# Kernel optimization log

Measured on AMD Instinct MI355X. Metric: run time of the kernel, lower is better.

The kernel has to match this reference:

```python
import jax, jax.numpy as jnp
import numpy as np

EPS = 1e-5
N_NODES = 100000
N_EDGES = 1600000
IN_F, HID_F, OUT_F = 128, 128, 64


def setup_inputs() -> dict:
    key = jax.random.key(0)
    ks = jax.random.split(key, 8)
    def xavier(k, fan_in, fan_out):
        lim = float(np.sqrt(6.0 / (fan_in + fan_out)))
        return jax.random.uniform(k, (fan_in, fan_out), jnp.float32, -lim, lim)
    return {
        "features": jax.random.normal(ks[0], (N_NODES, IN_F), jnp.float32),
        "src": jax.random.randint(ks[1], (N_EDGES,), 0, N_NODES, jnp.int64 if jax.config.jax_enable_x64 else jnp.int32),
        "dst": jax.random.randint(ks[2], (N_EDGES,), 0, N_NODES, jnp.int64 if jax.config.jax_enable_x64 else jnp.int32),
        "W_self1": xavier(ks[3], IN_F, HID_F),
        "W_neigh1": xavier(ks[4], IN_F, HID_F),
        "b1": jnp.zeros((HID_F,), jnp.float32),
        "gamma1": jnp.ones((HID_F,), jnp.float32),
        "beta1": jnp.zeros((HID_F,), jnp.float32),
        "W_self2": xavier(ks[5], HID_F, OUT_F),
        "W_neigh2": xavier(ks[6], HID_F, OUT_F),
        "b2": jnp.zeros((OUT_F,), jnp.float32),
        "gamma2": jnp.ones((OUT_F,), jnp.float32),
        "beta2": jnp.zeros((OUT_F,), jnp.float32),
    }


def _sage_conv(h, src, dst, W_self, W_neigh, b, n_nodes):
    # mean aggregation of source-node features onto destination nodes
    agg = jax.ops.segment_sum(h[src], dst, num_segments=n_nodes)   # [N, d]
    deg = jax.ops.segment_sum(jnp.ones_like(dst, dtype=h.dtype), dst, num_segments=n_nodes)
    h_neigh = agg / jnp.maximum(deg, 1.0)[:, None]                  # zero-degree -> 0
    return h @ W_self + h_neigh @ W_neigh + b


def _batchnorm(h, gamma, beta):
    # training-mode BatchNorm1d: batch stats over node dim, biased variance
    mu = jnp.mean(h, axis=0)
    var = jnp.mean(jnp.square(h - mu), axis=0)
    return (h - mu) * jax.lax.rsqrt(var + EPS) * gamma + beta


def reference(features, src, dst, W_self1, W_neigh1, b1, gamma1, beta1,
              W_self2, W_neigh2, b2, gamma2, beta2):
    n = features.shape[0]
    h = _sage_conv(features, src, dst, W_self1, W_neigh1, b1, n)
    h = jax.nn.relu(_batchnorm(h, gamma1, beta1))
    h = _sage_conv(h, src, dst, W_self2, W_neigh2, b2, n)
    return _batchnorm(h, gamma2, beta2)
```

## Files before the change

kernel.cpp:

```cpp
#include <hip/hip_runtime.h>

#define EPS_BN 1e-5f
#define BINSHIFT 9
#define BINW 512
#define P_EPB 8192
#define LDS_CAP 10240
#define NREP 32

typedef __attribute__((ext_vector_type(8))) short short8;
typedef __attribute__((ext_vector_type(4))) float f32x4;

__device__ __forceinline__ unsigned short f2bf(float x) {
    unsigned int u = __float_as_uint(x);
    u += 0x7fffu + ((u >> 16) & 1u);
    return (unsigned short)(u >> 16);
}
__device__ __forceinline__ float bf2f(unsigned short h) {
    return __uint_as_float(((unsigned int)h) << 16);
}
__device__ __forceinline__ float bflo(unsigned u) { return __uint_as_float(u << 16); }
__device__ __forceinline__ float bfhi(unsigned u) { return __uint_as_float(u & 0xffff0000u); }
__device__ __forceinline__ float i8lo(unsigned short u) { return (float)(signed char)(u & 0xff); }
__device__ __forceinline__ float i8hi(unsigned short u) { return (float)(signed char)(u >> 8); }

__device__ __forceinline__ void scan512(int* a, int t) {
    for (int off = 1; off < 512; off <<= 1) {
        int v = (t >= off) ? a[t - off] : 0;
        __syncthreads();
        a[t] += v;
        __syncthreads();
    }
}
__device__ __forceinline__ void scan256(int* a, int t) {
    for (int off = 1; off < 256; off <<= 1) {
        int v = (t >= off) ? a[t - off] : 0;
        __syncthreads();
        a[t] += v;
        __syncthreads();
    }
}

__global__ __launch_bounds__(256) void prep_kernel(
    const float* __restrict__ Ws1, const float* __restrict__ Wn1,
    const float* __restrict__ Ws2, const float* __restrict__ Wn2,
    unsigned short* __restrict__ W1f, unsigned short* __restrict__ W2f,
    const int* __restrict__ dst, int* __restrict__ counts, int E, int NB, int wB) {
    int tid = threadIdx.x;
    if (blockIdx.x < wB) {
        int i = blockIdx.x * 256 + tid;
        if (i < 128 * 256) {
            int j = i & 7, L = (i >> 3) & 63, c = (i >> 9) & 15, kk = i >> 13;
            int k = kk * 32 + (L >> 4) * 8 + j;
            int col = c * 16 + (L & 15);
            float v = (col < 128) ? Ws1[k * 128 + col] : Wn1[k * 128 + (col - 128)];
            W1f[i] = f2bf(v);
        } else {
            int idx = i - 128 * 256;
            if (idx < 128 * 128) {
                int j = idx & 7, L = (idx >> 3) & 63, c = (idx >> 9) & 7, kk = idx >> 12;
                int k = kk * 32 + (L >> 4) * 8 + j;
                int col = c * 16 + (L & 15);
                float v = (col < 64) ? Ws2[k * 64 + col] : Wn2[k * 64 + (col - 64)];
                W2f[idx] = f2bf(v);
            }
        }
    } else {
        __shared__ int hist[512];
        int blk = blockIdx.x - wB;
        int e0 = blk * P_EPB, e1 = min(e0 + P_EPB, E);
        for (int b = tid; b < 512; b += 256) hist[b] = 0;
        __syncthreads();
        for (int e = e0 + tid; e < e1; e += 256) atomicAdd(&hist[dst[e] >> BINSHIFT], 1);
        __syncthreads();
        for (int b = tid; b < NB; b += 256) counts[blk * NB + b] = hist[b];
    }
}

__global__ __launch_bounds__(256) void p2a(const int* __restrict__ counts,
                                           int* __restrict__ segrel,
                                           int* __restrict__ tot, int NB, int NBLK) {
    __shared__ int s[256];
    int b = blockIdx.x, t = threadIdx.x;
    int v = (t < NBLK) ? counts[t * NB + b] : 0;
    s[t] = v;
    __syncthreads();
    scan256(s, t);
    if (t < NBLK) segrel[t * NB + b] = s[t] - v;
    if (t == 255) tot[b] = s[255];
}

__global__ __launch_bounds__(512) void p3_scatter(const int* __restrict__ src,
                                                  const int* __restrict__ dst,
                                                  const int* __restrict__ segrel,
                                                  const int* __restrict__ tot,
                                                  unsigned* __restrict__ epack,
                                                  int E, int NB) {
    __shared__ unsigned lp[P_EPB];
    __shared__ int hist[512];
    __shared__ int sBase[513];
    __shared__ int cursor[512];
    __shared__ int bbase[512];
    int t = threadIdx.x;
    int blk = blockIdx.x;
    int e0 = blk * P_EPB, e1 = min(e0 + P_EPB, E), m = e1 - e0;
    int tv = (t < NB) ? tot[t] : 0;
    bbase[t] = tv;
    __syncthreads();
    scan512(bbase, t);
    bbase[t] -= tv;
    hist[t] = 0;
    __syncthreads();
    for (int e = e0 + t; e < e1; e += 512) atomicAdd(&hist[dst[e] >> BINSHIFT], 1);
    __syncthreads();
    int h = hist[t];
    scan512(hist, t);
    int excl = hist[t] - h;
    sBase[t] = excl;
    cursor[t] = excl;
    if (t == 0) sBase[512] = m;
    __syncthreads();
    for (int e = e0 + t; e < e1; e += 512) {
        int d = dst[e];
        int pos = atomicAdd(&cursor[d >> BINSHIFT], 1);
        lp[pos] = ((unsigned)src[e] << BINSHIFT) | ((unsigned)d & (BINW - 1));
    }
    __syncthreads();
    for (int i = t; i < m; i += 512) {
        int lo = 0, hi = NB;
        while (hi - lo > 1) {
            int mid = (lo + hi) >> 1;
            if (sBase[mid] <= i) lo = mid; else hi = mid;
        }
        epack[bbase[lo] + segrel[blk * NB + lo] + (i - sBase[lo])] = lp[i];
    }
}

__global__ __launch_bounds__(512) void p4_csr(const unsigned* __restrict__ epack,
                                              const int* __restrict__ tot,
                                              int* __restrict__ row_start,
                                              int* __restrict__ cntg,
                                              float* __restrict__ inv_deg,
                                              int* __restrict__ csr_src, int N, int NB) {
    __shared__ int ncnt[512];
    __shared__ int cursor[512];
    __shared__ int bb[512];
    __shared__ int lsrc[LDS_CAP];
    int t = threadIdx.x;
    int b = blockIdx.x;
    int tv = (t < NB) ? tot[t] : 0;
    bb[t] = tv;
    __syncthreads();
    scan512(bb, t);
    int e1 = bb[b];
    int e0 = bb[b] - tot[b];
    int m = e1 - e0;
    int nbase = b << BINSHIFT;
    int nn = min(N - nbase, BINW);
    ncnt[t] = 0;
    __syncthreads();
    for (int i = e0 + t; i < e1; i += 512)
        atomicAdd(&ncnt[epack[i] & (BINW - 1)], 1);
    __syncthreads();
    int c = ncnt[t];
    scan512(ncnt, t);
    int excl = ncnt[t] - c;
    if (t < nn) {
        int node = nbase + t;
        row_start[node] = e0 + excl;
        cntg[node] = c;
        inv_deg[node] = 1.0f / fmaxf((float)c, 1.0f);
    }
    cursor[t] = excl;
    __syncthreads();
    for (int i = e0 + t; i < e1; i += 512) {
        unsigned v = epack[i];
        int pos = atomicAdd(&cursor[v & (BINW - 1)], 1);
        if (pos < LDS_CAP) lsrc[pos] = (int)(v >> BINSHIFT);
    }
    __syncthreads();
    int mm = min(m, LDS_CAP);
    for (int i = t; i < mm; i += 512) csr_src[e0 + i] = lsrc[i];
}

template <int MT, int MSELF, bool SELFBF, bool FUSEBN, bool AFP32>
__global__ __launch_bounds__(256) void gemm_dual(const unsigned short* __restrict__ Ab,
                                                 const float* __restrict__ Af,
                                                 const unsigned short* __restrict__ Wf,
                                                 float* __restrict__ YselfF,
                                                 unsigned short* __restrict__ YselfB,
                                                 signed char* __restrict__ Ynb8,
                                                 float* __restrict__ scl, int N,
                                                 const float* __restrict__ sums,
                                                 const float* __restrict__ gamma,
                                                 const float* __restrict__ beta,
                                                 float invN) {
    constexpr int K = 128;
    constexpr int NCT = MT / 16;
    constexpr int KS = K / 32;
    constexpr int MNB = MT - MSELF;
    constexpr int CSELF = MSELF / 16;
    __shared__ unsigned short Bl[KS * NCT * 64 * 8];
    __shared__ float ssc[128], ssh[128];

    for (int i = threadIdx.x; i < KS * NCT * 64; i += 256)
        ((short8*)Bl)[i] = ((const short8*)Wf)[i];
    if (FUSEBN && threadIdx.x < 128) {
        int c = threadIdx.x;
        float su = 0.f, sq = 0.f;
        for (int r = 0; r < NREP; r++) {
            su += sums[r * 256 + c];
            sq += sums[r * 256 + 128 + c];
        }
        float mu = su * invN;
        float var = sq * invN - mu * mu;
        float sc = gamma[c] * rsqrtf(var + EPS_BN);
        ssc[c] = sc;
        ssh[c] = beta[c] - mu * sc;
    }
    __syncthreads();

    int wv = threadIdx.x >> 6, lane = threadIdx.x & 63;
    int row0 = blockIdx.x * 128 + wv * 32;
    int m = lane & 15, quad = lane >> 4;

    short8 afrag[2][KS];
#pragma unroll
    for (int t = 0; t < 2; t++) {
        int arow = row0 + t * 16 + m;
        if (arow >= N) arow = N - 1;
#pragma unroll
        for (int kk = 0; kk < KS; kk++) {
            short8 raw;
            if (AFP32) {
                const float* ap = Af + (size_t)arow * K + quad * 8 + kk * 32;
                f32x4 a = *(const f32x4*)ap;
                f32x4 b = *(const f32x4*)(ap + 4);
#pragma unroll
                for (int j = 0; j < 4; j++) {
                    raw[j] = (short)f2bf(a[j]);
                    raw[4 + j] = (short)f2bf(b[j]);
                }
            } else {
                raw = *(const short8*)(Ab + (size_t)arow * K + quad * 8 + kk * 32);
            }
            if (FUSEBN) {
#pragma unroll
                for (int j = 0; j < 8; j++) {
                    int c = kk * 32 + quad * 8 + j;
                    float f = bf2f((unsigned short)raw[j]) * ssc[c] + ssh[c];
                    raw[j] = (short)f2bf(fmaxf(f, 0.f));
                }
            }
            afrag[t][kk] = raw;
        }
    }

    f32x4 acc[2][NCT];
#pragma unroll
    for (int t = 0; t < 2; t++)
        for (int c = 0; c < NCT; c++)
            for (int j = 0; j < 4; j++) acc[t][c][j] = 0.f;

#pragma unroll
    for (int kk = 0; kk < KS; kk++) {
#pragma unroll
        for (int c = 0; c < NCT; c++) {
            short8 bfrag = *(const short8*)&Bl[((kk * NCT + c) * 64 + lane) * 8];
#pragma unroll
            for (int t = 0; t < 2; t++)
                acc[t][c] = __builtin_amdgcn_mfma_f32_16x16x32_bf16(afrag[t][kk], bfrag,
                                                                    acc[t][c], 0, 0, 0);
        }
    }

#pragma unroll
    for (int t = 0; t < 2; t++) {
#pragma unroll
        for (int c = 0; c < CSELF; c++) {
            int colg = c * 16 + m;
#pragma unroll
            for (int r = 0; r < 4; r++) {
                int row = row0 + t * 16 + quad * 4 + r;
                if (row < N) {
                    float v = acc[t][c][r];
                    if (SELFBF)
                        YselfB[(size_t)row * MSELF + colg] = f2bf(v);
                    else
                        YselfF[(size_t)row * MSELF + colg] = v;
                }
            }
        }
#pragma unroll
        for (int r = 0; r < 4; r++) {
            float mx = 0.f;
#pragma unroll
            for (int c = CSELF; c < NCT; c++) mx = fmaxf(mx, fabsf(acc[t][c][r]));
#pragma unroll
            for (int off = 1; off < 16; off <<= 1) mx = fmaxf(mx, __shfl_xor(mx, off));
            int row = row0 + t * 16 + quad * 4 + r;
            float qs = 127.0f / fmaxf(mx, 1e-30f);
            if (row < N) {
                if (m == 0) scl[row] = mx * (1.0f / 127.0f);
#pragma unroll
                for (int c = CSELF; c < NCT; c++) {
                    int colg = c * 16 + m;
                    int q = __float2int_rn(acc[t][c][r] * qs);
                    Ynb8[(size_t)row * MNB + (colg - MSELF)] = (signed char)q;
                }
            }
        }
    }
}

__global__ __launch_bounds__(256) void agg_row128(const unsigned int* __restrict__ Sb,
                                                  const unsigned short* __restrict__ Tq,
                                                  const float* __restrict__ scl,
                                                  const int* __restrict__ row_start,
                                                  const int* __restrict__ cnt,
                                                  const float* __restrict__ inv_deg,
                                                  const int* __restrict__ csr_src,
                                                  const float* __restrict__ bias,
                                                  unsigned int* __restrict__ Out,
                                                  float* __restrict__ sums,
                                                  int N, int totalWaves) {
    int wv = threadIdx.x >> 6, lane = threadIdx.x & 63;
    int c = lane * 2;
    float bs0 = bias[c], bs1 = bias[c + 1];
    float S0 = 0.f, S1 = 0.f, Q0 = 0.f, Q1 = 0.f;

    int n = blockIdx.x * 4 + wv;
    int pStart = 0, pEc = 0, pIv = 0;
    float pInv = 0.f;
    if (n < N) {
        pStart = row_start[n];
        pEc = cnt[n];
        pInv = inv_deg[n];
        if (pEc > 0) pIv = csr_src[pStart + min(lane, min(pEc, 64) - 1)];
    }
    for (; n < N; n += totalWaves) {
        int start = pStart, ec = pEc, iv = pIv;
        float inv = pInv;
        unsigned su = Sb[(size_t)n * 64 + lane];
        int n2 = n + totalWaves;
        if (n2 < N) {
            pStart = row_start[n2];
            pEc = cnt[n2];
            pInv = inv_deg[n2];
            if (pEc > 0) pIv = csr_src[pStart + min(lane, min(pEc, 64) - 1)];
        }
        float a0 = 0.f, a1 = 0.f;
        for (int base = 0; base < ec; base += 64) {
            int ecc = min(ec - base, 64);
            if (base) iv = csr_src[start + base + min(lane, ecc - 1)];
            int e = 0;
            for (; e + 16 <= ecc; e += 16) {
                unsigned short u[16];
                float sc[16];
#pragma unroll
                for (int j = 0; j < 16; j++) {
                    int s = __builtin_amdgcn_readlane(iv, e + j);
                    u[j] = Tq[(size_t)s * 64 + lane];
                    sc[j] = scl[s];
                }
#pragma unroll
                for (int j = 0; j < 16; j++) {
                    a0 += sc[j] * i8lo(u[j]);
                    a1 += sc[j] * i8hi(u[j]);
                }
            }
            if (e + 8 <= ecc) {
                unsigned short u[8];
                float sc[8];
#pragma unroll
                for (int j = 0; j < 8; j++) {
                    int s = __builtin_amdgcn_readlane(iv, e + j);
                    u[j] = Tq[(size_t)s * 64 + lane];
                    sc[j] = scl[s];
                }
#pragma unroll
                for (int j = 0; j < 8; j++) {
                    a0 += sc[j] * i8lo(u[j]);
                    a1 += sc[j] * i8hi(u[j]);
                }
                e += 8;
            }
            if (e < ecc) {
                int r = ecc - e;
                unsigned short u[8];
                float sc[8];
#pragma unroll
                for (int j = 0; j < 8; j++) {
                    int s = __builtin_amdgcn_readlane(iv, min(e + j, ecc - 1));
                    u[j] = Tq[(size_t)s * 64 + lane];
                    sc[j] = scl[s];
                }
#pragma unroll
                for (int j = 0; j < 8; j++) {
                    if (j < r) {
                        a0 += sc[j] * i8lo(u[j]);
                        a1 += sc[j] * i8hi(u[j]);
                    }
                }
            }
        }
        float h0 = bflo(su) + a0 * inv + bs0;
        float h1 = bfhi(su) + a1 * inv + bs1;
        Out[(size_t)n * 64 + lane] = (unsigned)f2bf(h0) | ((unsigned)f2bf(h1) << 16);
        S0 += h0; Q0 += h0 * h0;
        S1 += h1; Q1 += h1 * h1;
    }
    __shared__ float ls[256];
    ls[threadIdx.x] = 0.f;
    __syncthreads();
    atomicAdd(&ls[c], S0);
    atomicAdd(&ls[c + 1], S1);
    atomicAdd(&ls[128 + c], Q0);
    atomicAdd(&ls[129 + c], Q1);
    __syncthreads();
    float* dstS = sums + (size_t)(blockIdx.x & (NREP - 1)) * 256;
    atomicAdd(&dstS[threadIdx.x], ls[threadIdx.x]);
}

__global__ __launch_bounds__(256) void agg_row64(const unsigned short* __restrict__ Tq,
                                                 const float* __restrict__ scl,
                                                 const int* __restrict__ row_start,
                                                 const int* __restrict__ cnt,
                                                 const float* __restrict__ inv_deg,
                                                 const int* __restrict__ csr_src,
                                                 const float* __restrict__ bias,
                                                 float* Self, float* __restrict__ sums,
                                                 int N, int totalWaves) {
    int wv = threadIdx.x >> 6, lane = threadIdx.x & 63;
    int g = lane >> 5, h = lane & 31;
    int c = h * 2;
    float bs0 = bias[c], bs1 = bias[c + 1];
    float S0 = 0.f, S1 = 0.f, Q0 = 0.f, Q1 = 0.f;

    int n = blockIdx.x * 4 + wv;
    int pStart = 0, pEc = 0, pIv = 0;
    if (n < N) {
        pStart = row_start[n];
        pEc = cnt[n];
        if (pEc > 0) pIv = csr_src[pStart + min(lane, min(pEc, 64) - 1)];
    }
    for (; n < N; n += totalWaves) {
        int start = pStart, ec = pEc, iv = pIv;
        float inv = inv_deg[n];
        int n2 = n + totalWaves;
        if (n2 < N) {
            pStart = row_start[n2];
            pEc = cnt[n2];
            if (pEc > 0) pIv = csr_src[pStart + min(lane, min(pEc, 64) - 1)];
        }
        float a0 = 0.f, a1 = 0.f;
        for (int base = 0; base < ec; base += 64) {
            int ecc = min(ec - base, 64);
            if (base) iv = csr_src[start + base + min(lane, ecc - 1)];
            int e = 0;
            for (; e + 8 <= ecc; e += 8) {
                unsigned short u[4];
                float sc[4];
#pragma unroll
                for (int j = 0; j < 4; j++) {
                    int s0 = __builtin_amdgcn_readlane(iv, e + 2 * j);
                    int s1 = __builtin_amdgcn_readlane(iv, e + 2 * j + 1);
                    int sg = g ? s1 : s0;
                    u[j] = Tq[(size_t)sg * 32 + h];
                    sc[j] = scl[sg];
                }
#pragma unroll
                for (int j = 0; j < 4; j++) {
                    a0 += sc[j] * i8lo(u[j]);
                    a1 += sc[j] * i8hi(u[j]);
                }
            }
            if (e < ecc) {
                int r = ecc - e;
                unsigned short u[4];
                float sc[4];
#pragma unroll
                for (int j = 0; j < 4; j++) {
                    int s0 = __builtin_amdgcn_readlane(iv, min(e + 2 * j, ecc - 1));
                    int s1 = __builtin_amdgcn_readlane(iv, min(e + 2 * j + 1, ecc - 1));
                    int sg = g ? s1 : s0;
                    u[j] = Tq[(size_t)sg * 32 + h];
                    sc[j] = scl[sg];
                }
#pragma unroll
                for (int j = 0; j < 4; j++) {
                    bool ok = (2 * j + g) < r;
                    a0 += ok ? sc[j] * i8lo(u[j]) : 0.f;
                    a1 += ok ? sc[j] * i8hi(u[j]) : 0.f;
                }
            }
        }
        a0 += __shfl_xor(a0, 32);
        a1 += __shfl_xor(a1, 32);
        if (g == 0) {
            size_t off = (size_t)n * 64 + c;
            float h0 = Self[off] + a0 * inv + bs0;
            float h1 = Self[off + 1] + a1 * inv + bs1;
            Self[off] = h0;
            Self[off + 1] = h1;
            S0 += h0; Q0 += h0 * h0;
            S1 += h1; Q1 += h1 * h1;
        }
    }
    __shared__ float ls[128];
    if (threadIdx.x < 128) ls[threadIdx.x] = 0.f;
    __syncthreads();
    if (g == 0) {
        atomicAdd(&ls[c], S0);
        atomicAdd(&ls[c + 1], S1);
        atomicAdd(&ls[64 + c], Q0);
        atomicAdd(&ls[65 + c], Q1);
    }
    __syncthreads();
    if (threadIdx.x < 128) {
        float* dstS = sums + (size_t)(blockIdx.x & (NREP - 1)) * 128;
        atomicAdd(&dstS[threadIdx.x], ls[threadIdx.x]);
    }
}

__global__ __launch_bounds__(256) void bn_apply_f64(float* H, const float* __restrict__ sums,
                                                    const float* __restrict__ gamma,
                                                    const float* __restrict__ beta,
                                                    int N, float invN) {
    __shared__ float ss[128];
    int tid = threadIdx.x;
    if (tid < 64) {
        float su = 0.f, sq = 0.f;
        for (int r = 0; r < NREP; r++) {
            su += sums[r * 128 + tid];
            sq += sums[r * 128 + 64 + tid];
        }
        float mu = su * invN;
        float var = sq * invN - mu * mu;
        float sc = gamma[tid] * rsqrtf(var + EPS_BN);
        ss[tid] = sc;
        ss[64 + tid] = beta[tid] - mu * sc;
    }
    __syncthreads();
    int total4 = N * 16;
    float4* H4 = (float4*)H;
    for (int i = blockIdx.x * 256 + threadIdx.x; i < total4; i += 256 * gridDim.x) {
        int c0 = (i * 4) & 63;
        float4 v = H4[i];
        float4 sc = *(const float4*)&ss[c0];
        float4 sh = *(const float4*)&ss[64 + c0];
        v.x = v.x * sc.x + sh.x;
        v.y = v.y * sc.y + sh.y;
        v.z = v.z * sc.z + sh.z;
        v.w = v.w * sc.w + sh.w;
        H4[i] = v;
    }
}

extern "C" void kernel_launch(void* const* d_in, const int* in_sizes, int n_in,
                              void* d_out, int out_size, void* d_ws, size_t ws_size,
                              hipStream_t stream) {
    const float* X = (const float*)d_in[0];
    const int* src = (const int*)d_in[1];
    const int* dst = (const int*)d_in[2];
    const float* Wself1 = (const float*)d_in[3];
    const float* Wneigh1 = (const float*)d_in[4];
    const float* b1 = (const float*)d_in[5];
    const float* g1 = (const float*)d_in[6];
    const float* be1 = (const float*)d_in[7];
    const float* Wself2 = (const float*)d_in[8];
    const float* Wneigh2 = (const float*)d_in[9];
    const float* b2 = (const float*)d_in[10];
    const float* g2 = (const float*)d_in[11];
    const float* be2 = (const float*)d_in[12];
    float* out = (float*)d_out;

    const int N = in_sizes[0] / 128;
    const int E = in_sizes[1];
    const int NB = (N + BINW - 1) >> BINSHIFT;
    const int NBLK = (E + P_EPB - 1) / P_EPB;

    char* p = (char*)d_ws;
    auto carve = [&](size_t bytes) {
        char* r = p;
        p += (bytes + 255) & ~(size_t)255;
        return r;
    };
    float* sums1 = (float*)carve((size_t)NREP * 256 * 4);
    float* sums2 = (float*)carve((size_t)NREP * 128 * 4);
    size_t zero_bytes = (size_t)(p - (char*)d_ws);
    int* counts = (int*)carve((size_t)NBLK * NB * 4);
    int* segrel = (int*)carve((size_t)NBLK * NB * 4);
    int* tot = (int*)carve((size_t)NB * 4);
    unsigned* epack = (unsigned*)carve((size_t)E * 4);
    int* csr_src = (int*)carve((size_t)E * 4);
    int* row_start = (int*)carve((size_t)N * 4);
    int* cntg = (int*)carve((size_t)N * 4);
    float* inv_deg = (float*)carve((size_t)N * 4);
    unsigned short* W1f = (unsigned short*)carve(128 * 256 * 2);
    unsigned short* W2f = (unsigned short*)carve(128 * 128 * 2);
    unsigned short* bufS = (unsigned short*)carve((size_t)N * 128 * 2);
    signed char* Tq1 = (signed char*)carve((size_t)N * 128);
    float* scl1 = (float*)carve((size_t)N * 4);
    signed char* Tq2 = (signed char*)carve((size_t)N * 64);
    float* scl2 = (float*)carve((size_t)N * 4);
    unsigned short* h1b = (unsigned short*)carve((size_t)N * 128 * 2);

    hipMemsetAsync(d_ws, 0, zero_bytes, stream);

    const int wB = 192;
    const float invN = 1.0f / (float)N;
    prep_kernel<<<wB + NBLK, 256, 0, stream>>>(Wself1, Wneigh1, Wself2, Wneigh2, W1f, W2f,
                                               dst, counts, E, NB, wB);
    p2a<<<NB, 256, 0, stream>>>(counts, segrel, tot, NB, NBLK);
    p3_scatter<<<NBLK, 512, 0, stream>>>(src, dst, segrel, tot, epack, E, NB);
    p4_csr<<<NB, 512, 0, stream>>>(epack, tot, row_start, cntg, inv_deg, csr_src, N, NB);

    int ggrid = (N + 127) / 128;
    gemm_dual<256, 128, true, false, true><<<ggrid, 256, 0, stream>>>(
        nullptr, X, W1f, nullptr, bufS, Tq1, scl1, N, nullptr, nullptr, nullptr, 0.f);
    agg_row128<<<2048, 256, 0, stream>>>(
        (const unsigned int*)bufS, (const unsigned short*)Tq1, scl1, row_start, cntg,
        inv_deg, csr_src, b1, (unsigned int*)h1b, sums1, N, 8192);

    gemm_dual<128, 64, false, true, false><<<ggrid, 256, 0, stream>>>(
        h1b, nullptr, W2f, out, nullptr, Tq2, scl2, N, sums1, g1, be1, invN);
    agg_row64<<<2048, 256, 0, stream>>>(
        (const unsigned short*)Tq2, scl2, row_start, cntg, inv_deg, csr_src, b2, out,
        sums2, N, 8192);
    bn_apply_f64<<<2048, 256, 0, stream>>>(out, sums2, g2, be2, N, invN);
}
```

Before: 361.3 us.

## Split gemm_dual waves by column half and read weights from global memory

Each block now covers 64 rows instead of 128. Pairs of waves share a 32-row tile, and each wave computes only the self half or only the neighbour half of the output columns. This halves the accumulator registers per wave and removes the per-block staging of the full weight matrix into LDS along with its barrier. Weight fragments are instead loaded straight from global memory, relying on cache hits. In exchange, every A fragment is loaded and converted twice (once per column-half wave), and the grid doubles.

```diff
diff --git a/kernel.cpp b/kernel.cpp
--- a/kernel.cpp
+++ b/kernel.cpp
@@ -196,31 +196,33 @@
                                                  float invN) {
     constexpr int K = 128;
     constexpr int NCT = MT / 16;
+    constexpr int NCTW = NCT / 2;
     constexpr int KS = K / 32;
     constexpr int MNB = MT - MSELF;
-    constexpr int CSELF = MSELF / 16;
-    __shared__ unsigned short Bl[KS * NCT * 64 * 8];
+    static_assert(MSELF * 2 == MT, "col-half split requires MSELF == MT/2");
     __shared__ float ssc[128], ssh[128];
 
-    for (int i = threadIdx.x; i < KS * NCT * 64; i += 256)
-        ((short8*)Bl)[i] = ((const short8*)Wf)[i];
-    if (FUSEBN && threadIdx.x < 128) {
-        int c = threadIdx.x;
-        float su = 0.f, sq = 0.f;
-        for (int r = 0; r < NREP; r++) {
-            su += sums[r * 256 + c];
-            sq += sums[r * 256 + 128 + c];
-        }
-        float mu = su * invN;
-        float var = sq * invN - mu * mu;
-        float sc = gamma[c] * rsqrtf(var + EPS_BN);
-        ssc[c] = sc;
-        ssh[c] = beta[c] - mu * sc;
-    }
-    __syncthreads();
+    if constexpr (FUSEBN) {
+        if (threadIdx.x < 128) {
+            int c = threadIdx.x;
+            float su = 0.f, sq = 0.f;
+            for (int r = 0; r < NREP; r++) {
+                su += sums[r * 256 + c];
+                sq += sums[r * 256 + 128 + c];
+            }
+            float mu = su * invN;
+            float var = sq * invN - mu * mu;
+            float sc = gamma[c] * rsqrtf(var + EPS_BN);
+            ssc[c] = sc;
+            ssh[c] = beta[c] - mu * sc;
+        }
+        __syncthreads();
+    }
 
     int wv = threadIdx.x >> 6, lane = threadIdx.x & 63;
-    int row0 = blockIdx.x * 128 + wv * 32;
+    int ch = wv & 1;
+    int rt = wv >> 1;
+    int row0 = blockIdx.x * 64 + rt * 32;
     int m = lane & 15, quad = lane >> 4;
 
     short8 afrag[2][KS];
@@ -255,57 +257,65 @@
         }
     }
 
-    f32x4 acc[2][NCT];
+    f32x4 acc[2][NCTW];
 #pragma unroll
     for (int t = 0; t < 2; t++)
-        for (int c = 0; c < NCT; c++)
-            for (int j = 0; j < 4; j++) acc[t][c][j] = 0.f;
-
+        for (int ci = 0; ci < NCTW; ci++)
+            for (int j = 0; j < 4; j++) acc[t][ci][j] = 0.f;
+
+    const short8* Bf = (const short8*)Wf;
+    int cbase = ch * NCTW;
 #pragma unroll
     for (int kk = 0; kk < KS; kk++) {
 #pragma unroll
-        for (int c = 0; c < NCT; c++) {
-            short8 bfrag = *(const short8*)&Bl[((kk * NCT + c) * 64 + lane) * 8];
+        for (int ci = 0; ci < NCTW; ci++) {
+            short8 bfrag = Bf[(kk * NCT + cbase + ci) * 64 + lane];
 #pragma unroll
             for (int t = 0; t < 2; t++)
-                acc[t][c] = __builtin_amdgcn_mfma_f32_16x16x32_bf16(afrag[t][kk], bfrag,
-                                                                    acc[t][c], 0, 0, 0);
-        }
-    }
-
-#pragma unroll
-    for (int t = 0; t < 2; t++) {
-#pragma unroll
-        for (int c = 0; c < CSELF; c++) {
-            int colg = c * 16 + m;
+                acc[t][ci] = __builtin_amdgcn_mfma_f32_16x16x32_bf16(afrag[t][kk], bfrag,
+                                                                     acc[t][ci], 0, 0, 0);
+        }
+    }
+
+    if (ch == 0) {
+#pragma unroll
+        for (int t = 0; t < 2; t++) {
+#pragma unroll
+            for (int ci = 0; ci < NCTW; ci++) {
+                int colg = ci * 16 + m;
+#pragma unroll
+                for (int r = 0; r < 4; r++) {
+                    int row = row0 + t * 16 + quad * 4 + r;
+                    if (row < N) {
+                        float v = acc[t][ci][r];
+                        if (SELFBF)
+                            YselfB[(size_t)row * MSELF + colg] = f2bf(v);
+                        else
+                            YselfF[(size_t)row * MSELF + colg] = v;
+                    }
+                }
+            }
+        }
+    } else {
+#pragma unroll
+        for (int t = 0; t < 2; t++) {
 #pragma unroll
             for (int r = 0; r < 4; r++) {
+                float mx = 0.f;
+#pragma unroll
+                for (int ci = 0; ci < NCTW; ci++) mx = fmaxf(mx, fabsf(acc[t][ci][r]));
+#pragma unroll
+                for (int off = 1; off < 16; off <<= 1) mx = fmaxf(mx, __shfl_xor(mx, off));
                 int row = row0 + t * 16 + quad * 4 + r;
+                float qs = 127.0f / fmaxf(mx, 1e-30f);
                 if (row < N) {
-                    float v = acc[t][c][r];
-                    if (SELFBF)
-                        YselfB[(size_t)row * MSELF + colg] = f2bf(v);
-                    else
-                        YselfF[(size_t)row * MSELF + colg] = v;
-                }
-            }
-        }
-#pragma unroll
-        for (int r = 0; r < 4; r++) {
-            float mx = 0.f;
-#pragma unroll
-            for (int c = CSELF; c < NCT; c++) mx = fmaxf(mx, fabsf(acc[t][c][r]));
-#pragma unroll
-            for (int off = 1; off < 16; off <<= 1) mx = fmaxf(mx, __shfl_xor(mx, off));
-            int row = row0 + t * 16 + quad * 4 + r;
-            float qs = 127.0f / fmaxf(mx, 1e-30f);
-            if (row < N) {
-                if (m == 0) scl[row] = mx * (1.0f / 127.0f);
-#pragma unroll
-                for (int c = CSELF; c < NCT; c++) {
-                    int colg = c * 16 + m;
-                    int q = __float2int_rn(acc[t][c][r] * qs);
-                    Ynb8[(size_t)row * MNB + (colg - MSELF)] = (signed char)q;
+                    if (m == 0) scl[row] = mx * (1.0f / 127.0f);
+#pragma unroll
+                    for (int ci = 0; ci < NCTW; ci++) {
+                        int colg = ci * 16 + m;
+                        int q = __float2int_rn(acc[t][ci][r] * qs);
+                        Ynb8[(size_t)row * MNB + colg] = (signed char)q;
+                    }
                 }
             }
         }
@@ -615,7 +625,7 @@
     p3_scatter<<<NBLK, 512, 0, stream>>>(src, dst, segrel, tot, epack, E, NB);
     p4_csr<<<NB, 512, 0, stream>>>(epack, tot, row_start, cntg, inv_deg, csr_src, N, NB);
 
-    int ggrid = (N + 127) / 128;
+    int ggrid = (N + 63) / 64;
     gemm_dual<256, 128, true, false, true><<<ggrid, 256, 0, stream>>>(
         nullptr, X, W1f, nullptr, bufS, Tq1, scl1, N, nullptr, nullptr, nullptr, 0.f);
     agg_row128<<<2048, 256, 0, stream>>>(
```

New measurement: 338.3 us. -6.4%, faster.
